# Kernel optimization log

Measured on AMD Instinct MI355X. Metric: run time of the kernel, lower is better.

Reference implementation:

```python
import jax, jax.numpy as jnp
import numpy as np

D_IN, D_HID, D_OUT = 4096, 8192, 1000


def setup_inputs() -> dict:
    key = jax.random.key(0)
    ks = jax.random.split(key, 7)
    s1 = 1.0 / np.sqrt(D_IN)
    s2 = 1.0 / np.sqrt(D_HID)
    return {
        "x": jax.random.normal(ks[0], (D_IN,), dtype=jnp.float32),
        "W1": jax.random.normal(ks[1], (D_HID, D_IN), dtype=jnp.float32) * s1,
        "b1": jax.random.normal(ks[2], (D_HID,), dtype=jnp.float32) * 0.01,
        "W2": jax.random.normal(ks[3], (D_HID, D_HID), dtype=jnp.float32) * s2,
        "b2": jax.random.normal(ks[4], (D_HID,), dtype=jnp.float32) * 0.01,
        "W3": jax.random.normal(ks[5], (D_OUT, D_HID), dtype=jnp.float32) * s2,
        "b3": jax.random.normal(ks[6], (D_OUT,), dtype=jnp.float32) * 0.01,
    }


def reference(x, W1, b1, W2, b2, W3, b3):
    # layer 1: matvec + bias + square activation (h_relu is x*x)
    h = W1 @ x + b1
    h = h * h
    # layer 2
    h = W2 @ h + b2
    h = h * h
    # layer 3 (no activation)
    return W3 @ h + b3
```

## Files before the change

### kernel.cpp

```cpp
#include <hip/hip_runtime.h>
#include <hip/hip_bf16.h>


__global__ __launch_bounds__(256) void matvec_rowblock(
    const float* __restrict__ W,
    const float* __restrict__ x,
    const float* __restrict__ bias,
    float* __restrict__ y,
    int K, int do_square)
{
    const int row = blockIdx.x;
    const int tid = threadIdx.x;
    const float4* __restrict__ W4 = (const float4*)(W + (size_t)row * (size_t)K);
    const float4* __restrict__ x4 = (const float4*)x;
    const int K4 = K >> 2;

    float acc = 0.0f;
    for (int i = tid; i < K4; i += 256) {
        float4 w = W4[i];
        float4 v = x4[i];
        acc += w.x * v.x + w.y * v.y + w.z * v.z + w.w * v.w;
    }

    #pragma unroll
    for (int off = 32; off > 0; off >>= 1)
        acc += __shfl_down(acc, off, 64);

    __shared__ float wsum[4];
    const int wave = tid >> 6;
    const int lane = tid & 63;
    if (lane == 0) wsum[wave] = acc;
    __syncthreads();

    if (tid == 0) {
        float s = (wsum[0] + wsum[1]) + (wsum[2] + wsum[3]);
        s += bias[row];
        if (do_square) s = s * s;
        y[row] = s;
    }
}

extern "C" void kernel_launch(void* const* d_in, const int* in_sizes, int n_in,
                              void* d_out, int out_size, void* d_ws, size_t ws_size,
                              hipStream_t stream) {
    const float* x  = (const float*)d_in[0];
    const float* W1 = (const float*)d_in[1];
    const float* b1 = (const float*)d_in[2];
    const float* W2 = (const float*)d_in[3];
    const float* b2 = (const float*)d_in[4];
    const float* W3 = (const float*)d_in[5];
    const float* b3 = (const float*)d_in[6];
    float* out = (float*)d_out;

    const int D_IN = 4096, D_HID = 8192, D_OUT = 1000;

    float* h1 = (float*)d_ws;
    float* h2 = h1 + D_HID;

    matvec_rowblock<<<D_HID, 256, 0, stream>>>(W1, x, b1, h1, D_IN, 1);
    matvec_rowblock<<<D_HID, 256, 0, stream>>>(W2, h1, b2, h2, D_HID, 1);
    matvec_rowblock<<<D_OUT, 256, 0, stream>>>(W3, h2, b3, out, D_HID, 0);
}
```

Measured before the change: 454.5 us.

## Compute two rows per block with compile-time K and fully unrolled loop

Each block now computes two output rows, sharing each loaded x vector across both rows and halving the block count. K becomes a template parameter so the inner loop is fully unrolled, which gives more independent loads in flight per thread. The kernel stays bandwidth-bound on streaming the weights, so the gain comes mainly from better memory-level parallelism and fewer blocks. The cost is higher register use per thread.

```diff
diff --git a/kernel.cpp b/kernel.cpp
--- a/kernel.cpp
+++ b/kernel.cpp
@@ -2,41 +2,53 @@
 #include <hip/hip_bf16.h>
 
 
-__global__ __launch_bounds__(256) void matvec_rowblock(
+template<int K>
+__global__ __launch_bounds__(256) void matvec2row(
     const float* __restrict__ W,
     const float* __restrict__ x,
     const float* __restrict__ bias,
     float* __restrict__ y,
-    int K, int do_square)
+    int do_square)
 {
-    const int row = blockIdx.x;
-    const int tid = threadIdx.x;
-    const float4* __restrict__ W4 = (const float4*)(W + (size_t)row * (size_t)K);
+    constexpr int K4   = K / 4;
+    constexpr int ITER = K4 / 256;
+    const int row0 = blockIdx.x * 2;
+    const int tid  = threadIdx.x;
+
+    const float4* __restrict__ Wa = (const float4*)(W + (size_t)row0 * K);
+    const float4* __restrict__ Wb = (const float4*)(W + (size_t)(row0 + 1) * K);
     const float4* __restrict__ x4 = (const float4*)x;
-    const int K4 = K >> 2;
 
-    float acc = 0.0f;
-    for (int i = tid; i < K4; i += 256) {
-        float4 w = W4[i];
-        float4 v = x4[i];
-        acc += w.x * v.x + w.y * v.y + w.z * v.z + w.w * v.w;
+    float acc0 = 0.0f, acc1 = 0.0f;
+    #pragma unroll
+    for (int it = 0; it < ITER; ++it) {
+        const int i = tid + it * 256;
+        float4 v  = x4[i];
+        float4 wa = Wa[i];
+        float4 wb = Wb[i];
+        acc0 += wa.x * v.x + wa.y * v.y + wa.z * v.z + wa.w * v.w;
+        acc1 += wb.x * v.x + wb.y * v.y + wb.z * v.z + wb.w * v.w;
     }
 
     #pragma unroll
-    for (int off = 32; off > 0; off >>= 1)
-        acc += __shfl_down(acc, off, 64);
+    for (int off = 32; off > 0; off >>= 1) {
+        acc0 += __shfl_down(acc0, off, 64);
+        acc1 += __shfl_down(acc1, off, 64);
+    }
 
-    __shared__ float wsum[4];
+    __shared__ float s0[4], s1[4];
     const int wave = tid >> 6;
-    const int lane = tid & 63;
-    if (lane == 0) wsum[wave] = acc;
+    if ((tid & 63) == 0) { s0[wave] = acc0; s1[wave] = acc1; }
     __syncthreads();
 
     if (tid == 0) {
-        float s = (wsum[0] + wsum[1]) + (wsum[2] + wsum[3]);
-        s += bias[row];
-        if (do_square) s = s * s;
-        y[row] = s;
+        float r0 = (s0[0] + s0[1]) + (s0[2] + s0[3]);
+        float r1 = (s1[0] + s1[1]) + (s1[2] + s1[3]);
+        r0 += bias[row0];
+        r1 += bias[row0 + 1];
+        if (do_square) { r0 = r0 * r0; r1 = r1 * r1; }
+        y[row0]     = r0;
+        y[row0 + 1] = r1;
     }
 }
 
@@ -52,12 +64,12 @@
     const float* b3 = (const float*)d_in[6];
     float* out = (float*)d_out;
 
-    const int D_IN = 4096, D_HID = 8192, D_OUT = 1000;
+    const int D_HID = 8192, D_OUT = 1000;
 
     float* h1 = (float*)d_ws;
     float* h2 = h1 + D_HID;
 
-    matvec_rowblock<<<D_HID, 256, 0, stream>>>(W1, x, b1, h1, D_IN, 1);
-    matvec_rowblock<<<D_HID, 256, 0, stream>>>(W2, h1, b2, h2, D_HID, 1);
-    matvec_rowblock<<<D_OUT, 256, 0, stream>>>(W3, h2, b3, out, D_HID, 0);
+    matvec2row<4096><<<D_HID / 2, 256, 0, stream>>>(W1, x, b1, h1, 1);
+    matvec2row<8192><<<D_HID / 2, 256, 0, stream>>>(W2, h1, b2, h2, 1);
+    matvec2row<8192><<<D_OUT / 2, 256, 0, stream>>>(W3, h2, b3, out, 0);
 }
```

After: 448.2 us. No clear change (-1.4%).
